# Performance work log

Hardware: AMD Instinct MI355X
Metric: run time of the kernel (lower is better)

Reference implementation:

```python
import jax, jax.numpy as jnp
import numpy as np

N_HEADS = 8
WINDOW = 7

def _conv1x1(x, W, b):
    # x: [B,H,W,C]; 1x1 conv == per-pixel matmul
    return jnp.einsum('bhwc,cd->bhwd', x, W) + b

def _to_heads(t, nh):
    # [B,H,W,C] -> channels-first reshape [B, nh, C//nh, H*W] (matches tf transpose+reshape)
    B, H, W, C = t.shape
    return jnp.transpose(t, (0, 3, 1, 2)).reshape(B, nh, C // nh, H * W)

def setup_inputs() -> dict:
    key = jax.random.key(0)
    ks = jax.random.split(key, 8)
    B, H, W, C = 2, 56, 56, 256
    x = jax.random.normal(ks[0], (B, H, W, C), dtype=jnp.float32)
    s = 1.0 / np.sqrt(C)
    Wq = jax.random.normal(ks[1], (C, C), dtype=jnp.float32) * s
    bq = jnp.zeros((C,), dtype=jnp.float32)
    Wk = jax.random.normal(ks[2], (C, C), dtype=jnp.float32) * s
    bk = jnp.zeros((C,), dtype=jnp.float32)
    Wv = jax.random.normal(ks[3], (C, C), dtype=jnp.float32) * s
    bv = jnp.zeros((C,), dtype=jnp.float32)
    # original initializes gamma to 0 (output == x); use small nonzero so the
    # attention path is observable in outputs/grads
    gamma = jax.random.normal(ks[4], (1,), dtype=jnp.float32) * 0.1
    return {"x": x, "Wq": Wq, "bq": bq, "Wk": Wk, "bk": bk, "Wv": Wv, "bv": bv, "gamma": gamma}

def reference(x, Wq, bq, Wk, bk, Wv, bv, gamma):
    B, H, W, C = x.shape
    p = WINDOW // 2
    xp = jnp.pad(x, ((0, 0), (p, p), (p, p), (0, 0)), mode='reflect')  # [B,Hp,Wp,C]
    q = _to_heads(_conv1x1(x, Wq, bq), N_HEADS)    # [B,nh,dk,HW]
    k = _to_heads(_conv1x1(xp, Wk, bk), N_HEADS)   # [B,nh,dk,HpWp]
    v = _to_heads(_conv1x1(xp, Wv, bv), N_HEADS)   # [B,nh,dk,HpWp]
    energy = jnp.einsum('bhdq,bhdk->bhqk', q, k)   # [B,nh,HW,HpWp]
    attn = jax.nn.softmax(energy, axis=-1)
    out = jnp.einsum('bhdk,bhqk->bhdq', v, attn)   # [B,nh,dk,HW]
    out = out.reshape(B, C, H, W).transpose(0, 2, 3, 1)
    return gamma * out + x
```

## Files before the change

### kernel.cpp

```cpp
#include <hip/hip_runtime.h>

typedef unsigned short u16;
typedef float f32x4 __attribute__((ext_vector_type(4)));
typedef short bf16x8 __attribute__((ext_vector_type(8)));
typedef short bf16x4 __attribute__((ext_vector_type(4)));

__device__ __forceinline__ u16 f2bf(float f) {
    unsigned u = __float_as_uint(f);
    u = (u + 0x7FFFu + ((u >> 16) & 1u)) >> 16;
    return (u16)u;
}

#define LOG2E 1.4426950408889634f

#if __has_builtin(__builtin_amdgcn_exp2f)
__device__ __forceinline__ float exp2_fast(float x) { return __builtin_amdgcn_exp2f(x); }
#else
__device__ __forceinline__ float exp2_fast(float x) { return __expf(x * 0.6931471805599453f); }
#endif

__device__ __forceinline__ unsigned pack2bf(float a, float b) {
    unsigned ua = __float_as_uint(a) + 0x8000u;
    unsigned ub = __float_as_uint(b) + 0x8000u;
#if __has_builtin(__builtin_amdgcn_perm)
    return __builtin_amdgcn_perm(ub, ua, 0x07060302u);
#else
    return ((ua >> 16) & 0xFFFFu) | (ub & 0xFFFF0000u);
#endif
}

#if __has_builtin(__builtin_amdgcn_cvt_pk_bf16_f32)
typedef __bf16 bf2_t __attribute__((ext_vector_type(2)));
__device__ __forceinline__ unsigned cvtpk(float a, float b) {
    bf2_t r = __builtin_amdgcn_cvt_pk_bf16_f32(a, b);
    return __builtin_bit_cast(unsigned, r);
}
#else
__device__ __forceinline__ unsigned cvtpk(float a, float b) { return pack2bf(a, b); }
#endif

__device__ __forceinline__ bf16x4 bc4(uint2 u) { return __builtin_bit_cast(bf16x4, u); }
__device__ __forceinline__ bf16x8 bc8(uint4 u) { return __builtin_bit_cast(bf16x8, u); }

#if __has_builtin(__builtin_amdgcn_global_load_lds)
typedef const __attribute__((address_space(1))) void* as1cv;
typedef __attribute__((address_space(3))) void* as3v;
__device__ __forceinline__ void dma16(const void* g, void* lds_base, int lane) {
    __builtin_amdgcn_global_load_lds((as1cv)g, (as3v)lds_base, 16, 0, 0);
}
#else
__device__ __forceinline__ void dma16(const void* g, void* lds_base, int lane) {
    *(uint4*)((char*)lds_base + lane * 16) = *(const uint4*)g;
}
#endif

#if __has_builtin(__builtin_amdgcn_mfma_f32_16x16x16bf16_1k)
__device__ __forceinline__ f32x4 pv_mfma(bf16x4 a, bf16x4 b, f32x4 c) {
    return __builtin_amdgcn_mfma_f32_16x16x16bf16_1k(a, b, c, 0, 0, 0);
}
#elif __has_builtin(__builtin_amdgcn_mfma_f32_16x16x16_bf16)
__device__ __forceinline__ f32x4 pv_mfma(bf16x4 a, bf16x4 b, f32x4 c) {
    return __builtin_amdgcn_mfma_f32_16x16x16_bf16(a, b, c, 0, 0, 0);
}
#else
__device__ __forceinline__ f32x4 pv_mfma(bf16x4 a, bf16x4 b, f32x4 c) {
    bf16x8 a8 = {a[0], a[1], a[2], a[3], 0, 0, 0, 0};
    bf16x8 b8 = {b[0], b[1], b[2], b[3], 0, 0, 0, 0};
    return __builtin_amdgcn_mfma_f32_16x16x32_bf16(a8, b8, c, 0, 0, 0);
}
#endif

#define BB 2
#define HH 56
#define CC 256
#define NH 8
#define DK 32
#define SQ 3136
#define HP 62
#define SK 3844
#define VT_STRIDE 3856

#define WS_Q    0
#define WS_K    1605632
#define WS_VT   3573760
#define WS_LB   5548032

#define NZERO_F4 413952

#define BSTR 40
__global__ __launch_bounds__(256, 4) void proj_kernel(const float* __restrict__ x,
                                                      const float* __restrict__ Wq,
                                                      const float* __restrict__ Wk,
                                                      const float* __restrict__ Wv,
                                                      const float* __restrict__ bq,
                                                      const float* __restrict__ bk,
                                                      const float* __restrict__ bv,
                                                      u16* __restrict__ qout,
                                                      u16* __restrict__ kout,
                                                      u16* __restrict__ vtout,
                                                      float* __restrict__ out,
                                                      float* __restrict__ lbuf) {
    __shared__ __align__(16) u16 Bl[128 * BSTR];

    int mode  = blockIdx.y;
    int nz    = blockIdx.z;
    int mbase = blockIdx.x * 64;
    int tid = threadIdx.x;

    {
        int gid = ((blockIdx.z * 3 + blockIdx.y) * 121 + blockIdx.x) * 256 + tid;
        const int n_out4 = (SQ * BB * CC) / 4;
        for (int i = gid; i < NZERO_F4; i += 726 * 256) {
            if (i < n_out4) *(float4*)&out[i * 4] = (float4){0.f, 0.f, 0.f, 0.f};
            else            *(float4*)&lbuf[(i - n_out4) * 4] = (float4){0.f, 0.f, 0.f, 0.f};
        }
    }

    int M = (mode == 0) ? (BB * SQ) : (BB * SK);
    if (mbase >= M) return;
    int wave = tid >> 6, lane = tid & 63, quad = lane >> 4, l16 = lane & 15;

    const float* W = (mode == 0) ? Wq : ((mode == 1) ? Wk : Wv);
    const float* bias = (mode == 0) ? bq : ((mode == 1) ? bk : bv);
    float wscale = (mode == 0) ? LOG2E : 1.0f;

    int m_a = mbase + wave * 16 + l16;
    if (m_a >= M) m_a = M - 1;
    int xrow;
    if (mode == 0) {
        xrow = m_a;
    } else {
        int b = (m_a >= SK) ? 1 : 0;
        int sp = m_a - b * SK;
        int hp = sp / HP, wp = sp - hp * HP;
        int hs = hp - 3; hs = hs < 0 ? -hs : (hs >= HH ? 110 - hs : hs);
        int ws_ = wp - 3; ws_ = ws_ < 0 ? -ws_ : (ws_ >= HH ? 110 - ws_ : ws_);
        xrow = b * SQ + hs * HH + ws_;
    }
    const float* xr = x + (size_t)xrow * 256;

    int kq = tid >> 3;
    int cb = (tid & 7) * 16;

    f32x4 acc[8];
#pragma unroll
    for (int i = 0; i < 8; i++) acc[i] = (f32x4){0.f, 0.f, 0.f, 0.f};

    float4 wreg[4];
    auto wload = [&](int s) {
        const float* p = W + (size_t)(s * 32 + kq) * 256 + nz * 128 + cb;
        wreg[0] = *(const float4*)&p[0];
        wreg[1] = *(const float4*)&p[4];
        wreg[2] = *(const float4*)&p[8];
        wreg[3] = *(const float4*)&p[12];
    };
    auto wwrite = [&]() {
#pragma unroll
        for (int i = 0; i < 16; i++) {
            float v = ((const float*)wreg)[i] * wscale;
            Bl[(cb + i) * BSTR + kq] = f2bf(v);
        }
    };

    wload(0);
    for (int s = 0; s < 8; ++s) {
        int kk = s * 32;
        wwrite();
        __syncthreads();
        if (s < 7) wload(s + 1);
        float4 f0 = *(const float4*)&xr[kk + quad * 8];
        float4 f1 = *(const float4*)&xr[kk + quad * 8 + 4];
        uint4 aw = (uint4){pack2bf(f0.x, f0.y), pack2bf(f0.z, f0.w),
                           pack2bf(f1.x, f1.y), pack2bf(f1.z, f1.w)};
        bf16x8 afrag = bc8(aw);
#pragma unroll
        for (int nt = 0; nt < 8; nt++) {
            bf16x8 bfrag = *(const bf16x8*)&Bl[(nt * 16 + l16) * BSTR + quad * 8];
            acc[nt] = __builtin_amdgcn_mfma_f32_16x16x32_bf16(afrag, bfrag, acc[nt], 0, 0, 0);
        }
        __syncthreads();
    }

    int mrow_base = mbase + wave * 16 + quad * 4;
    if (mode == 2) {
#pragma unroll
        for (int nt = 0; nt < 8; nt++) {
            int c = nz * 128 + nt * 16 + l16;
            float bvv = bias[c];
#pragma unroll
            for (int p = 0; p < 4; p += 2) {
                int m = mrow_base + p;
                if (m + 1 < M) {
                    int bb = (m >= SK) ? 1 : 0;
                    int kp = m - bb * SK;
                    unsigned pk = pack2bf(acc[nt][p] + bvv, acc[nt][p + 1] + bvv);
                    *(unsigned*)&vtout[(size_t)(bb * 256 + c) * VT_STRIDE + kp] = pk;
                }
            }
        }
    } else {
#pragma unroll
        for (int r = 0; r < 4; r++) {
            int m = mrow_base + r;
            if (m >= M) continue;
#pragma unroll
            for (int nt = 0; nt < 8; nt++) {
                int c = nz * 128 + nt * 16 + l16;
                float v = acc[nt][r] + bias[c] * ((mode == 0) ? LOG2E : 1.0f);
                u16 hv = f2bf(v);
                if (mode == 0) qout[((size_t)m << 8) + c] = hv;
                else           kout[((size_t)m << 8) + c] = hv;
            }
        }
    }
}

__global__ __launch_bounds__(256) void attn_kernel(const u16* __restrict__ qb,
                                                   const u16* __restrict__ kb,
                                                   const u16* __restrict__ vtb,
                                                   float* __restrict__ out,
                                                   float* __restrict__ lbuf) {
    __shared__ __align__(16) u16 S[16384];

    int tid = threadIdx.x;
    int wave = tid >> 6, lane = tid & 63, quad = lane >> 4, l16 = lane & 15;
    int qs = wave & 1, th = wave >> 1;
    int bh = blockIdx.y;
    int b = bh >> 3, h = bh & 7;
    int half = blockIdx.z;
    int qsub = blockIdx.x * 64 + qs * 32;
    int rounds = half ? 15 : 16;

    bf16x8 qf0 = *(const bf16x8*)&qb[((size_t)(b * SQ + qsub + l16) << 8) + h * 32 + quad * 8];
    bf16x8 qf1 = *(const bf16x8*)&qb[((size_t)(b * SQ + qsub + 16 + l16) << 8) + h * 32 + quad * 8];

    const u16* kg = kb + ((size_t)(b * SK) << 8) + h * 32;
    const u16* vg = vtb + (size_t)(b * 256 + h * 32) * VT_STRIDE;

    f32x4 o00{0.f,0.f,0.f,0.f}, o01{0.f,0.f,0.f,0.f};
    f32x4 o10{0.f,0.f,0.f,0.f}, o11{0.f,0.f,0.f,0.f};
    f32x4 l0{0.f,0.f,0.f,0.f},  l1{0.f,0.f,0.f,0.f};

    short ov = (l16 == 0) ? (short)0x3F80 : (short)0;
    bf16x4 ones4 = {ov, ov, ov, ov};

    auto stage = [&](int r_ch, int buf) {
        u16* base = &S[buf * 8192];
        int kbase = (half * 16 + r_ch) * 128;
#pragma unroll
        for (int i = 0; i < 2; ++i) {
            int g = wave + i * 4;
            int grow = kbase + g * 16 + (lane & 15);
            if (grow > SK - 1) grow = SK - 1;
            dma16(kg + ((size_t)grow << 8) + (lane >> 4) * 8, base + g * 512, lane);
            int col = kbase + (2 * g + (lane >> 5)) * 8;
            if (col > VT_STRIDE - 8) col = VT_STRIDE - 8;
            dma16(vg + (size_t)(lane & 31) * VT_STRIDE + col, base + 4096 + g * 512, lane);
        }
    };

    stage(0, 0);
    __syncthreads();
    stage(1, 1);

    for (int r = 0; r < 16; ++r) {
        if (r < rounds) {
            const u16* Kl = &S[(r & 1) * 8192];
            const u16* Vl = Kl + 4096;
            int ch = half * 16 + r;
            bool tail = (ch == 30);
#pragma unroll
            for (int tt = 0; tt < 4; ++tt) {
                int t = th * 4 + tt;
                bf16x8 kf = *(const bf16x8*)&Kl[t * 512 + ((quad << 4) + l16) * 8];
                f32x4 e0 = __builtin_amdgcn_mfma_f32_16x16x32_bf16(kf, qf0, (f32x4){0.f,0.f,0.f,0.f}, 0, 0, 0);
                f32x4 e1 = __builtin_amdgcn_mfma_f32_16x16x32_bf16(kf, qf1, (f32x4){0.f,0.f,0.f,0.f}, 0, 0, 0);
                float p0[4], p1[4];
                if (tail) {
                    int kb0 = ch * 128 + t * 16 + quad * 4;
#pragma unroll
                    for (int j = 0; j < 4; ++j) {
                        bool valid = (kb0 + j) < SK;
                        p0[j] = valid ? exp2_fast(e0[j]) : 0.f;
                        p1[j] = valid ? exp2_fast(e1[j]) : 0.f;
                    }
                } else {
#pragma unroll
                    for (int j = 0; j < 4; ++j) {
                        p0[j] = exp2_fast(e0[j]);
                        p1[j] = exp2_fast(e1[j]);
                    }
                }
                bf16x4 pa0 = bc4((uint2){cvtpk(p0[0], p0[1]), cvtpk(p0[2], p0[3])});
                bf16x4 pa1 = bc4((uint2){cvtpk(p1[0], p1[1]), cvtpk(p1[2], p1[3])});
                int vbase = ((2 * t + (quad >> 1)) << 8) + (quad & 1) * 4;
                uint2 w0 = *(const uint2*)&Vl[vbase + l16 * 8];
                uint2 w1 = *(const uint2*)&Vl[vbase + (16 + l16) * 8];
                bf16x4 vb0 = bc4(w0), vb1 = bc4(w1);
                o00 = pv_mfma(pa0, vb0, o00);
                o01 = pv_mfma(pa0, vb1, o01);
                o10 = pv_mfma(pa1, vb0, o10);
                o11 = pv_mfma(pa1, vb1, o11);
                l0  = pv_mfma(pa0, ones4, l0);
                l1  = pv_mfma(pa1, ones4, l1);
            }
        }
        __syncthreads();
        if (r + 2 < rounds) stage(r + 2, r & 1);
    }

    float* mg = (float*)&S[0];
    int slot = (qs * 64 + lane) * 24;
    if (th == 1) {
        *(f32x4*)&mg[slot + 0]  = o00;
        *(f32x4*)&mg[slot + 4]  = o01;
        *(f32x4*)&mg[slot + 8]  = o10;
        *(f32x4*)&mg[slot + 12] = o11;
        *(f32x4*)&mg[slot + 16] = l0;
        *(f32x4*)&mg[slot + 20] = l1;
    }
    __syncthreads();
    if (th == 0) {
        o00 += *(const f32x4*)&mg[slot + 0];
        o01 += *(const f32x4*)&mg[slot + 4];
        o10 += *(const f32x4*)&mg[slot + 8];
        o11 += *(const f32x4*)&mg[slot + 12];
        l0  += *(const f32x4*)&mg[slot + 16];
        l1  += *(const f32x4*)&mg[slot + 20];

#pragma unroll
        for (int r2 = 0; r2 < 4; ++r2) {
            int q0 = qsub + quad * 4 + r2;
            int q1 = q0 + 16;
            size_t base0 = (size_t)(b * SQ + q0) * 256 + h * 32;
            size_t base1 = (size_t)(b * SQ + q1) * 256 + h * 32;
            atomicAdd(&out[base0 + l16],      o00[r2]);
            atomicAdd(&out[base0 + 16 + l16], o01[r2]);
            atomicAdd(&out[base1 + l16],      o10[r2]);
            atomicAdd(&out[base1 + 16 + l16], o11[r2]);
            if (l16 == 0) {
                atomicAdd(&lbuf[(b * SQ + q0) * 8 + h], l0[r2]);
                atomicAdd(&lbuf[(b * SQ + q1) * 8 + h], l1[r2]);
            }
        }
    }
}

__global__ __launch_bounds__(256) void finalize_kernel(const float* __restrict__ x,
                                                       const float* __restrict__ gammap,
                                                       const float* __restrict__ lbuf,
                                                       float* __restrict__ out) {
    int gid = blockIdx.x * 256 + threadIdx.x;
    int row = gid >> 6;
    int c4  = (gid & 63) << 2;
    int h   = c4 >> 5;
    float g = gammap[0];
    float linv = g / lbuf[row * 8 + h];
    size_t base = (size_t)row * 256 + c4;
    float4 o = *(const float4*)&out[base];
    float4 xv = *(const float4*)&x[base];
    o.x = o.x * linv + xv.x;
    o.y = o.y * linv + xv.y;
    o.z = o.z * linv + xv.z;
    o.w = o.w * linv + xv.w;
    *(float4*)&out[base] = o;
}

extern "C" void kernel_launch(void* const* d_in, const int* in_sizes, int n_in,
                              void* d_out, int out_size, void* d_ws, size_t ws_size,
                              hipStream_t stream) {
    const float* x     = (const float*)d_in[0];
    const float* Wq    = (const float*)d_in[1];
    const float* bq    = (const float*)d_in[2];
    const float* Wk    = (const float*)d_in[3];
    const float* bk    = (const float*)d_in[4];
    const float* Wv    = (const float*)d_in[5];
    const float* bv    = (const float*)d_in[6];
    const float* gamma = (const float*)d_in[7];
    float* out = (float*)d_out;

    u16* ws   = (u16*)d_ws;
    u16* qbuf = ws + WS_Q;
    u16* kbuf = ws + WS_K;
    u16* vtb  = ws + WS_VT;
    float* lbuf = (float*)(ws + WS_LB);

    proj_kernel<<<dim3(121, 3, 2), 256, 0, stream>>>(x, Wq, Wk, Wv, bq, bk, bv,
                                                     qbuf, kbuf, vtb, out, lbuf);
    attn_kernel<<<dim3(49, 16, 2), 256, 0, stream>>>(qbuf, kbuf, vtb, out, lbuf);
    finalize_kernel<<<1568, 256, 0, stream>>>(x, gamma, lbuf, out);
}
```

Measured before the change: 157.0 us.

## Have each attention wave handle all 64 queries over a quarter of the key tiles

Restructures the attention kernel so each of the four waves covers all 64 queries of the block (four Q fragments) and a disjoint subset of the key tiles, instead of 32 queries and half the key tiles. Each K fragment and V load from LDS is now reused across four query fragments, cutting LDS traffic per MFMA. In exchange it needs more accumulator registers (launch bounds now ask for 4 blocks per CU) and a two-stage LDS reduction across the four waves at the end. The weight-write lambda in the projection kernel is also inlined, with no change in behaviour.

```diff
diff --git a/kernel.cpp b/kernel.cpp
--- a/kernel.cpp
+++ b/kernel.cpp
@@ -154,18 +154,15 @@
         wreg[2] = *(const float4*)&p[8];
         wreg[3] = *(const float4*)&p[12];
     };
-    auto wwrite = [&]() {
+
+    wload(0);
+    for (int s = 0; s < 8; ++s) {
+        int kk = s * 32;
 #pragma unroll
         for (int i = 0; i < 16; i++) {
             float v = ((const float*)wreg)[i] * wscale;
             Bl[(cb + i) * BSTR + kq] = f2bf(v);
         }
-    };
-
-    wload(0);
-    for (int s = 0; s < 8; ++s) {
-        int kk = s * 32;
-        wwrite();
         __syncthreads();
         if (s < 7) wload(s + 1);
         float4 f0 = *(const float4*)&xr[kk + quad * 8];
@@ -215,31 +212,36 @@
     }
 }
 
-__global__ __launch_bounds__(256) void attn_kernel(const u16* __restrict__ qb,
-                                                   const u16* __restrict__ kb,
-                                                   const u16* __restrict__ vtb,
-                                                   float* __restrict__ out,
-                                                   float* __restrict__ lbuf) {
+__global__ __launch_bounds__(256, 4) void attn_kernel(const u16* __restrict__ qb,
+                                                      const u16* __restrict__ kb,
+                                                      const u16* __restrict__ vtb,
+                                                      float* __restrict__ out,
+                                                      float* __restrict__ lbuf) {
     __shared__ __align__(16) u16 S[16384];
 
     int tid = threadIdx.x;
-    int wave = tid >> 6, lane = tid & 63, quad = lane >> 4, l16 = lane & 15;
-    int qs = wave & 1, th = wave >> 1;
+    int th = tid >> 6, lane = tid & 63, quad = lane >> 4, l16 = lane & 15;
     int bh = blockIdx.y;
     int b = bh >> 3, h = bh & 7;
     int half = blockIdx.z;
-    int qsub = blockIdx.x * 64 + qs * 32;
+    int qsub = blockIdx.x * 64;
     int rounds = half ? 15 : 16;
 
-    bf16x8 qf0 = *(const bf16x8*)&qb[((size_t)(b * SQ + qsub + l16) << 8) + h * 32 + quad * 8];
-    bf16x8 qf1 = *(const bf16x8*)&qb[((size_t)(b * SQ + qsub + 16 + l16) << 8) + h * 32 + quad * 8];
+    bf16x8 qf[4];
+#pragma unroll
+    for (int i = 0; i < 4; ++i)
+        qf[i] = *(const bf16x8*)&qb[((size_t)(b * SQ + qsub + i * 16 + l16) << 8) + h * 32 + quad * 8];
 
     const u16* kg = kb + ((size_t)(b * SK) << 8) + h * 32;
     const u16* vg = vtb + (size_t)(b * 256 + h * 32) * VT_STRIDE;
 
-    f32x4 o00{0.f,0.f,0.f,0.f}, o01{0.f,0.f,0.f,0.f};
-    f32x4 o10{0.f,0.f,0.f,0.f}, o11{0.f,0.f,0.f,0.f};
-    f32x4 l0{0.f,0.f,0.f,0.f},  l1{0.f,0.f,0.f,0.f};
+    f32x4 o[4][2], lv[4];
+#pragma unroll
+    for (int i = 0; i < 4; ++i) {
+        o[i][0] = (f32x4){0.f,0.f,0.f,0.f};
+        o[i][1] = (f32x4){0.f,0.f,0.f,0.f};
+        lv[i]   = (f32x4){0.f,0.f,0.f,0.f};
+    }
 
     short ov = (l16 == 0) ? (short)0x3F80 : (short)0;
     bf16x4 ones4 = {ov, ov, ov, ov};
@@ -249,7 +251,7 @@
         int kbase = (half * 16 + r_ch) * 128;
 #pragma unroll
         for (int i = 0; i < 2; ++i) {
-            int g = wave + i * 4;
+            int g = th + i * 4;
             int grow = kbase + g * 16 + (lane & 15);
             if (grow > SK - 1) grow = SK - 1;
             dma16(kg + ((size_t)grow << 8) + (lane >> 4) * 8, base + g * 512, lane);
@@ -263,46 +265,46 @@
     __syncthreads();
     stage(1, 1);
 
-    for (int r = 0; r < 16; ++r) {
-        if (r < rounds) {
-            const u16* Kl = &S[(r & 1) * 8192];
-            const u16* Vl = Kl + 4096;
-            int ch = half * 16 + r;
-            bool tail = (ch == 30);
-#pragma unroll
-            for (int tt = 0; tt < 4; ++tt) {
-                int t = th * 4 + tt;
-                bf16x8 kf = *(const bf16x8*)&Kl[t * 512 + ((quad << 4) + l16) * 8];
-                f32x4 e0 = __builtin_amdgcn_mfma_f32_16x16x32_bf16(kf, qf0, (f32x4){0.f,0.f,0.f,0.f}, 0, 0, 0);
-                f32x4 e1 = __builtin_amdgcn_mfma_f32_16x16x32_bf16(kf, qf1, (f32x4){0.f,0.f,0.f,0.f}, 0, 0, 0);
-                float p0[4], p1[4];
-                if (tail) {
-                    int kb0 = ch * 128 + t * 16 + quad * 4;
-#pragma unroll
-                    for (int j = 0; j < 4; ++j) {
-                        bool valid = (kb0 + j) < SK;
-                        p0[j] = valid ? exp2_fast(e0[j]) : 0.f;
-                        p1[j] = valid ? exp2_fast(e1[j]) : 0.f;
-                    }
-                } else {
-#pragma unroll
-                    for (int j = 0; j < 4; ++j) {
-                        p0[j] = exp2_fast(e0[j]);
-                        p1[j] = exp2_fast(e1[j]);
-                    }
+    for (int r = 0; r < rounds; ++r) {
+        const u16* Kl = &S[(r & 1) * 8192];
+        const u16* Vl = Kl + 4096;
+        int ch = half * 16 + r;
+        bool tail = (ch == 30);
+#pragma unroll
+        for (int tt = 0; tt < 2; ++tt) {
+            int t = th + tt * 4;
+            bf16x8 kf = *(const bf16x8*)&Kl[t * 512 + ((quad << 4) + l16) * 8];
+            f32x4 e[4];
+#pragma unroll
+            for (int i = 0; i < 4; ++i)
+                e[i] = __builtin_amdgcn_mfma_f32_16x16x32_bf16(kf, qf[i], (f32x4){0.f,0.f,0.f,0.f}, 0, 0, 0);
+            bf16x4 pa[4];
+            if (tail) {
+                int kb0 = ch * 128 + t * 16 + quad * 4;
+#pragma unroll
+                for (int i = 0; i < 4; ++i) {
+                    float p0 = (kb0 + 0) < SK ? exp2_fast(e[i][0]) : 0.f;
+                    float p1 = (kb0 + 1) < SK ? exp2_fast(e[i][1]) : 0.f;
+                    float p2 = (kb0 + 2) < SK ? exp2_fast(e[i][2]) : 0.f;
+                    float p3 = (kb0 + 3) < SK ? exp2_fast(e[i][3]) : 0.f;
+                    pa[i] = bc4((uint2){cvtpk(p0, p1), cvtpk(p2, p3)});
                 }
-                bf16x4 pa0 = bc4((uint2){cvtpk(p0[0], p0[1]), cvtpk(p0[2], p0[3])});
-                bf16x4 pa1 = bc4((uint2){cvtpk(p1[0], p1[1]), cvtpk(p1[2], p1[3])});
-                int vbase = ((2 * t + (quad >> 1)) << 8) + (quad & 1) * 4;
-                uint2 w0 = *(const uint2*)&Vl[vbase + l16 * 8];
-                uint2 w1 = *(const uint2*)&Vl[vbase + (16 + l16) * 8];
-                bf16x4 vb0 = bc4(w0), vb1 = bc4(w1);
-                o00 = pv_mfma(pa0, vb0, o00);
-                o01 = pv_mfma(pa0, vb1, o01);
-                o10 = pv_mfma(pa1, vb0, o10);
-                o11 = pv_mfma(pa1, vb1, o11);
-                l0  = pv_mfma(pa0, ones4, l0);
-                l1  = pv_mfma(pa1, ones4, l1);
+            } else {
+#pragma unroll
+                for (int i = 0; i < 4; ++i) {
+                    pa[i] = bc4((uint2){cvtpk(exp2_fast(e[i][0]), exp2_fast(e[i][1])),
+                                        cvtpk(exp2_fast(e[i][2]), exp2_fast(e[i][3]))});
+                }
+            }
+            int vbase = ((2 * t + (quad >> 1)) << 8) + (quad & 1) * 4;
+            uint2 w0 = *(const uint2*)&Vl[vbase + l16 * 8];
+            uint2 w1 = *(const uint2*)&Vl[vbase + (16 + l16) * 8];
+            bf16x4 vb0 = bc4(w0), vb1 = bc4(w1);
+#pragma unroll
+            for (int i = 0; i < 4; ++i) {
+                o[i][0] = pv_mfma(pa[i], vb0, o[i][0]);
+                o[i][1] = pv_mfma(pa[i], vb1, o[i][1]);
+                lv[i]   = pv_mfma(pa[i], ones4, lv[i]);
             }
         }
         __syncthreads();
@@ -310,37 +312,56 @@
     }
 
     float* mg = (float*)&S[0];
-    int slot = (qs * 64 + lane) * 24;
-    if (th == 1) {
-        *(f32x4*)&mg[slot + 0]  = o00;
-        *(f32x4*)&mg[slot + 4]  = o01;
-        *(f32x4*)&mg[slot + 8]  = o10;
-        *(f32x4*)&mg[slot + 12] = o11;
-        *(f32x4*)&mg[slot + 16] = l0;
-        *(f32x4*)&mg[slot + 20] = l1;
-    }
-    __syncthreads();
-    if (th == 0) {
-        o00 += *(const f32x4*)&mg[slot + 0];
-        o01 += *(const f32x4*)&mg[slot + 4];
-        o10 += *(const f32x4*)&mg[slot + 8];
-        o11 += *(const f32x4*)&mg[slot + 12];
-        l0  += *(const f32x4*)&mg[slot + 16];
-        l1  += *(const f32x4*)&mg[slot + 20];
-
-#pragma unroll
-        for (int r2 = 0; r2 < 4; ++r2) {
-            int q0 = qsub + quad * 4 + r2;
-            int q1 = q0 + 16;
-            size_t base0 = (size_t)(b * SQ + q0) * 256 + h * 32;
-            size_t base1 = (size_t)(b * SQ + q1) * 256 + h * 32;
-            atomicAdd(&out[base0 + l16],      o00[r2]);
-            atomicAdd(&out[base0 + 16 + l16], o01[r2]);
-            atomicAdd(&out[base1 + l16],      o10[r2]);
-            atomicAdd(&out[base1 + 16 + l16], o11[r2]);
-            if (l16 == 0) {
-                atomicAdd(&lbuf[(b * SQ + q0) * 8 + h], l0[r2]);
-                atomicAdd(&lbuf[(b * SQ + q1) * 8 + h], l1[r2]);
+    {
+        int slot = ((th & 1) * 64 + lane) * 48;
+        if (th >= 2) {
+#pragma unroll
+            for (int i = 0; i < 4; ++i) {
+                *(f32x4*)&mg[slot + i * 8]     = o[i][0];
+                *(f32x4*)&mg[slot + i * 8 + 4] = o[i][1];
+                *(f32x4*)&mg[slot + 32 + i * 4] = lv[i];
+            }
+        }
+        __syncthreads();
+        if (th < 2) {
+#pragma unroll
+            for (int i = 0; i < 4; ++i) {
+                o[i][0] += *(const f32x4*)&mg[slot + i * 8];
+                o[i][1] += *(const f32x4*)&mg[slot + i * 8 + 4];
+                lv[i]   += *(const f32x4*)&mg[slot + 32 + i * 4];
+            }
+        }
+        __syncthreads();
+    }
+    {
+        int slot = lane * 48;
+        if (th == 1) {
+#pragma unroll
+            for (int i = 0; i < 4; ++i) {
+                *(f32x4*)&mg[slot + i * 8]     = o[i][0];
+                *(f32x4*)&mg[slot + i * 8 + 4] = o[i][1];
+                *(f32x4*)&mg[slot + 32 + i * 4] = lv[i];
+            }
+        }
+        __syncthreads();
+        if (th == 0) {
+#pragma unroll
+            for (int i = 0; i < 4; ++i) {
+                o[i][0] += *(const f32x4*)&mg[slot + i * 8];
+                o[i][1] += *(const f32x4*)&mg[slot + i * 8 + 4];
+                lv[i]   += *(const f32x4*)&mg[slot + 32 + i * 4];
+            }
+
+#pragma unroll
+            for (int i = 0; i < 4; ++i) {
+#pragma unroll
+                for (int r2 = 0; r2 < 4; ++r2) {
+                    int q = qsub + i * 16 + quad * 4 + r2;
+                    size_t base = (size_t)(b * SQ + q) * 256 + h * 32;
+                    atomicAdd(&out[base + l16],      o[i][0][r2]);
+                    atomicAdd(&out[base + 16 + l16], o[i][1][r2]);
+                    if (l16 == 0) atomicAdd(&lbuf[(b * SQ + q) * 8 + h], lv[i][r2]);
+                }
             }
         }
     }
```

After: 156.9 us. About the same (-0.0%).

## Load K/V straight to registers with double-buffering, drop LDS staging

Applied to the files above, without the earlier changes.

The projection kernel now writes V in a tiled layout of 16-key groups per head, so each lane can fetch its MFMA B-fragment directly with one 8-byte global load. The attention kernel drops the LDS double-buffered DMA staging and the per-round barriers. It instead prefetches K and V fragments for the next chunk into registers (A/B ping-pong) while computing the current one. This removes LDS traffic and synchronisation, but raises register pressure and relies on cache for K/V reuse across waves.

```diff
diff --git a/kernel.cpp b/kernel.cpp
--- a/kernel.cpp
+++ b/kernel.cpp
@@ -42,18 +42,6 @@
 __device__ __forceinline__ bf16x4 bc4(uint2 u) { return __builtin_bit_cast(bf16x4, u); }
 __device__ __forceinline__ bf16x8 bc8(uint4 u) { return __builtin_bit_cast(bf16x8, u); }
 
-#if __has_builtin(__builtin_amdgcn_global_load_lds)
-typedef const __attribute__((address_space(1))) void* as1cv;
-typedef __attribute__((address_space(3))) void* as3v;
-__device__ __forceinline__ void dma16(const void* g, void* lds_base, int lane) {
-    __builtin_amdgcn_global_load_lds((as1cv)g, (as3v)lds_base, 16, 0, 0);
-}
-#else
-__device__ __forceinline__ void dma16(const void* g, void* lds_base, int lane) {
-    *(uint4*)((char*)lds_base + lane * 16) = *(const uint4*)g;
-}
-#endif
-
 #if __has_builtin(__builtin_amdgcn_mfma_f32_16x16x16bf16_1k)
 __device__ __forceinline__ f32x4 pv_mfma(bf16x4 a, bf16x4 b, f32x4 c) {
     return __builtin_amdgcn_mfma_f32_16x16x16bf16_1k(a, b, c, 0, 0, 0);
@@ -78,11 +66,11 @@
 #define SQ 3136
 #define HP 62
 #define SK 3844
-#define VT_STRIDE 3856
+#define NTG 241
 
 #define WS_Q    0
 #define WS_K    1605632
-#define WS_VT   3573760
+#define WS_V3   3573760
 #define WS_LB   5548032
 
 #define NZERO_F4 413952
@@ -97,7 +85,7 @@
                                                       const float* __restrict__ bv,
                                                       u16* __restrict__ qout,
                                                       u16* __restrict__ kout,
-                                                      u16* __restrict__ vtout,
+                                                      u16* __restrict__ v3out,
                                                       float* __restrict__ out,
                                                       float* __restrict__ lbuf) {
     __shared__ __align__(16) u16 Bl[128 * BSTR];
@@ -154,18 +142,15 @@
         wreg[2] = *(const float4*)&p[8];
         wreg[3] = *(const float4*)&p[12];
     };
-    auto wwrite = [&]() {
+
+    wload(0);
+    for (int s = 0; s < 8; ++s) {
+        int kk = s * 32;
 #pragma unroll
         for (int i = 0; i < 16; i++) {
             float v = ((const float*)wreg)[i] * wscale;
             Bl[(cb + i) * BSTR + kq] = f2bf(v);
         }
-    };
-
-    wload(0);
-    for (int s = 0; s < 8; ++s) {
-        int kk = s * 32;
-        wwrite();
         __syncthreads();
         if (s < 7) wload(s + 1);
         float4 f0 = *(const float4*)&xr[kk + quad * 8];
@@ -186,6 +171,7 @@
 #pragma unroll
         for (int nt = 0; nt < 8; nt++) {
             int c = nz * 128 + nt * 16 + l16;
+            int hh = c >> 5, dk32 = c & 31;
             float bvv = bias[c];
 #pragma unroll
             for (int p = 0; p < 4; p += 2) {
@@ -193,8 +179,10 @@
                 if (m + 1 < M) {
                     int bb = (m >= SK) ? 1 : 0;
                     int kp = m - bb * SK;
+                    int tg = kp >> 4, ki = kp & 15;
                     unsigned pk = pack2bf(acc[nt][p] + bvv, acc[nt][p + 1] + bvv);
-                    *(unsigned*)&vtout[(size_t)(bb * 256 + c) * VT_STRIDE + kp] = pk;
+                    size_t addr = ((size_t)((bb * 8 + hh) * NTG + tg) << 9) + dk32 * 16 + ki;
+                    *(unsigned*)&v3out[addr] = pk;
                 }
             }
         }
@@ -217,10 +205,10 @@
 
 __global__ __launch_bounds__(256) void attn_kernel(const u16* __restrict__ qb,
                                                    const u16* __restrict__ kb,
-                                                   const u16* __restrict__ vtb,
+                                                   const u16* __restrict__ v3b,
                                                    float* __restrict__ out,
                                                    float* __restrict__ lbuf) {
-    __shared__ __align__(16) u16 S[16384];
+    __shared__ __align__(16) float mg[3072];
 
     int tid = threadIdx.x;
     int wave = tid >> 6, lane = tid & 63, quad = lane >> 4, l16 = lane & 15;
@@ -230,12 +218,13 @@
     int half = blockIdx.z;
     int qsub = blockIdx.x * 64 + qs * 32;
     int rounds = half ? 15 : 16;
+    int ch0 = half * 16;
 
     bf16x8 qf0 = *(const bf16x8*)&qb[((size_t)(b * SQ + qsub + l16) << 8) + h * 32 + quad * 8];
     bf16x8 qf1 = *(const bf16x8*)&qb[((size_t)(b * SQ + qsub + 16 + l16) << 8) + h * 32 + quad * 8];
 
-    const u16* kg = kb + ((size_t)(b * SK) << 8) + h * 32;
-    const u16* vg = vtb + (size_t)(b * 256 + h * 32) * VT_STRIDE;
+    const u16* kg  = kb + ((size_t)(b * SK) << 8) + h * 32;
+    const u16* vgp = v3b + ((size_t)((b * 8 + h) * NTG) << 9);
 
     f32x4 o00{0.f,0.f,0.f,0.f}, o01{0.f,0.f,0.f,0.f};
     f32x4 o10{0.f,0.f,0.f,0.f}, o11{0.f,0.f,0.f,0.f};
@@ -244,72 +233,90 @@
     short ov = (l16 == 0) ? (short)0x3F80 : (short)0;
     bf16x4 ones4 = {ov, ov, ov, ov};
 
-    auto stage = [&](int r_ch, int buf) {
-        u16* base = &S[buf * 8192];
-        int kbase = (half * 16 + r_ch) * 128;
-#pragma unroll
-        for (int i = 0; i < 2; ++i) {
-            int g = wave + i * 4;
-            int grow = kbase + g * 16 + (lane & 15);
-            if (grow > SK - 1) grow = SK - 1;
-            dma16(kg + ((size_t)grow << 8) + (lane >> 4) * 8, base + g * 512, lane);
-            int col = kbase + (2 * g + (lane >> 5)) * 8;
-            if (col > VT_STRIDE - 8) col = VT_STRIDE - 8;
-            dma16(vg + (size_t)(lane & 31) * VT_STRIDE + col, base + 4096 + g * 512, lane);
-        }
-    };
-
-    stage(0, 0);
-    __syncthreads();
-    stage(1, 1);
-
-    for (int r = 0; r < 16; ++r) {
-        if (r < rounds) {
-            const u16* Kl = &S[(r & 1) * 8192];
-            const u16* Vl = Kl + 4096;
-            int ch = half * 16 + r;
-            bool tail = (ch == 30);
-#pragma unroll
-            for (int tt = 0; tt < 4; ++tt) {
-                int t = th * 4 + tt;
-                bf16x8 kf = *(const bf16x8*)&Kl[t * 512 + ((quad << 4) + l16) * 8];
-                f32x4 e0 = __builtin_amdgcn_mfma_f32_16x16x32_bf16(kf, qf0, (f32x4){0.f,0.f,0.f,0.f}, 0, 0, 0);
-                f32x4 e1 = __builtin_amdgcn_mfma_f32_16x16x32_bf16(kf, qf1, (f32x4){0.f,0.f,0.f,0.f}, 0, 0, 0);
-                float p0[4], p1[4];
-                if (tail) {
-                    int kb0 = ch * 128 + t * 16 + quad * 4;
-#pragma unroll
-                    for (int j = 0; j < 4; ++j) {
-                        bool valid = (kb0 + j) < SK;
-                        p0[j] = valid ? exp2_fast(e0[j]) : 0.f;
-                        p1[j] = valid ? exp2_fast(e1[j]) : 0.f;
-                    }
-                } else {
-#pragma unroll
-                    for (int j = 0; j < 4; ++j) {
-                        p0[j] = exp2_fast(e0[j]);
-                        p1[j] = exp2_fast(e1[j]);
-                    }
-                }
-                bf16x4 pa0 = bc4((uint2){cvtpk(p0[0], p0[1]), cvtpk(p0[2], p0[3])});
-                bf16x4 pa1 = bc4((uint2){cvtpk(p1[0], p1[1]), cvtpk(p1[2], p1[3])});
-                int vbase = ((2 * t + (quad >> 1)) << 8) + (quad & 1) * 4;
-                uint2 w0 = *(const uint2*)&Vl[vbase + l16 * 8];
-                uint2 w1 = *(const uint2*)&Vl[vbase + (16 + l16) * 8];
-                bf16x4 vb0 = bc4(w0), vb1 = bc4(w1);
-                o00 = pv_mfma(pa0, vb0, o00);
-                o01 = pv_mfma(pa0, vb1, o01);
-                o10 = pv_mfma(pa1, vb0, o10);
-                o11 = pv_mfma(pa1, vb1, o11);
-                l0  = pv_mfma(pa0, ones4, l0);
-                l1  = pv_mfma(pa1, ones4, l1);
-            }
-        }
-        __syncthreads();
-        if (r + 2 < rounds) stage(r + 2, r & 1);
-    }
-
-    float* mg = (float*)&S[0];
+    auto kptr = [&](int ch, int tt) -> const uint4* {
+        int key = (ch * 8 + th * 4 + tt) * 16 + l16;
+        if (key > SK - 1) key = SK - 1;
+        return (const uint4*)&kg[((size_t)key << 8) + quad * 8];
+    };
+    auto vptr = [&](int ch, int tt, int hi) -> const uint2* {
+        int tg = ch * 8 + th * 4 + tt;
+        if (tg > NTG - 1) tg = NTG - 1;
+        return (const uint2*)&vgp[((size_t)tg << 9) + hi * 256 + l16 * 16 + quad * 4];
+    };
+
+    uint4 kA0, kA1, kA2, kA3, kB0, kB1, kB2, kB3;
+    uint2 vA0l, vA0h, vA1l, vA1h, vA2l, vA2h, vA3l, vA3h;
+    uint2 vB0l, vB0h, vB1l, vB1h, vB2l, vB2h, vB3l, vB3h;
+
+    auto loadA = [&](int ch) {
+        kA0 = *kptr(ch, 0); kA1 = *kptr(ch, 1); kA2 = *kptr(ch, 2); kA3 = *kptr(ch, 3);
+        vA0l = *vptr(ch, 0, 0); vA0h = *vptr(ch, 0, 1);
+        vA1l = *vptr(ch, 1, 0); vA1h = *vptr(ch, 1, 1);
+        vA2l = *vptr(ch, 2, 0); vA2h = *vptr(ch, 2, 1);
+        vA3l = *vptr(ch, 3, 0); vA3h = *vptr(ch, 3, 1);
+    };
+    auto loadB = [&](int ch) {
+        kB0 = *kptr(ch, 0); kB1 = *kptr(ch, 1); kB2 = *kptr(ch, 2); kB3 = *kptr(ch, 3);
+        vB0l = *vptr(ch, 0, 0); vB0h = *vptr(ch, 0, 1);
+        vB1l = *vptr(ch, 1, 0); vB1h = *vptr(ch, 1, 1);
+        vB2l = *vptr(ch, 2, 0); vB2h = *vptr(ch, 2, 1);
+        vB3l = *vptr(ch, 3, 0); vB3h = *vptr(ch, 3, 1);
+    };
+
+    auto compute_tt = [&](int ch, int tt, uint4 kreg, uint2 vlo, uint2 vhi) {
+        bf16x8 kf = bc8(kreg);
+        f32x4 e0 = __builtin_amdgcn_mfma_f32_16x16x32_bf16(kf, qf0, (f32x4){0.f,0.f,0.f,0.f}, 0, 0, 0);
+        f32x4 e1 = __builtin_amdgcn_mfma_f32_16x16x32_bf16(kf, qf1, (f32x4){0.f,0.f,0.f,0.f}, 0, 0, 0);
+        bf16x4 pa0, pa1;
+        if (ch == 30) {
+            int kb0 = (ch * 8 + th * 4 + tt) * 16 + quad * 4;
+            float p00 = (kb0 + 0) < SK ? exp2_fast(e0[0]) : 0.f;
+            float p01 = (kb0 + 1) < SK ? exp2_fast(e0[1]) : 0.f;
+            float p02 = (kb0 + 2) < SK ? exp2_fast(e0[2]) : 0.f;
+            float p03 = (kb0 + 3) < SK ? exp2_fast(e0[3]) : 0.f;
+            float p10 = (kb0 + 0) < SK ? exp2_fast(e1[0]) : 0.f;
+            float p11 = (kb0 + 1) < SK ? exp2_fast(e1[1]) : 0.f;
+            float p12 = (kb0 + 2) < SK ? exp2_fast(e1[2]) : 0.f;
+            float p13 = (kb0 + 3) < SK ? exp2_fast(e1[3]) : 0.f;
+            pa0 = bc4((uint2){cvtpk(p00, p01), cvtpk(p02, p03)});
+            pa1 = bc4((uint2){cvtpk(p10, p11), cvtpk(p12, p13)});
+        } else {
+            pa0 = bc4((uint2){cvtpk(exp2_fast(e0[0]), exp2_fast(e0[1])),
+                              cvtpk(exp2_fast(e0[2]), exp2_fast(e0[3]))});
+            pa1 = bc4((uint2){cvtpk(exp2_fast(e1[0]), exp2_fast(e1[1])),
+                              cvtpk(exp2_fast(e1[2]), exp2_fast(e1[3]))});
+        }
+        bf16x4 vb0 = bc4(vlo), vb1 = bc4(vhi);
+        o00 = pv_mfma(pa0, vb0, o00);
+        o01 = pv_mfma(pa0, vb1, o01);
+        o10 = pv_mfma(pa1, vb0, o10);
+        o11 = pv_mfma(pa1, vb1, o11);
+        l0  = pv_mfma(pa0, ones4, l0);
+        l1  = pv_mfma(pa1, ones4, l1);
+    };
+
+    auto computeA = [&](int ch) {
+        compute_tt(ch, 0, kA0, vA0l, vA0h);
+        compute_tt(ch, 1, kA1, vA1l, vA1h);
+        compute_tt(ch, 2, kA2, vA2l, vA2h);
+        compute_tt(ch, 3, kA3, vA3l, vA3h);
+    };
+    auto computeB = [&](int ch) {
+        compute_tt(ch, 0, kB0, vB0l, vB0h);
+        compute_tt(ch, 1, kB1, vB1l, vB1h);
+        compute_tt(ch, 2, kB2, vB2l, vB2h);
+        compute_tt(ch, 3, kB3, vB3l, vB3h);
+    };
+
+    loadA(ch0);
+    for (int r = 0; r < rounds; r += 2) {
+        if (r + 1 < rounds) loadB(ch0 + r + 1);
+        computeA(ch0 + r);
+        if (r + 1 >= rounds) break;
+        if (r + 2 < rounds) loadA(ch0 + r + 2);
+        computeB(ch0 + r + 1);
+    }
+
     int slot = (qs * 64 + lane) * 24;
     if (th == 1) {
         *(f32x4*)&mg[slot + 0]  = o00;
@@ -382,11 +389,11 @@
     u16* ws   = (u16*)d_ws;
     u16* qbuf = ws + WS_Q;
     u16* kbuf = ws + WS_K;
-    u16* vtb  = ws + WS_VT;
+    u16* v3b  = ws + WS_V3;
     float* lbuf = (float*)(ws + WS_LB);
 
     proj_kernel<<<dim3(121, 3, 2), 256, 0, stream>>>(x, Wq, Wk, Wv, bq, bk, bv,
-                                                     qbuf, kbuf, vtb, out, lbuf);
-    attn_kernel<<<dim3(49, 16, 2), 256, 0, stream>>>(qbuf, kbuf, vtb, out, lbuf);
+                                                     qbuf, kbuf, v3b, out, lbuf);
+    attn_kernel<<<dim3(49, 16, 2), 256, 0, stream>>>(qbuf, kbuf, v3b, out, lbuf);
     finalize_kernel<<<1568, 256, 0, stream>>>(x, gamma, lbuf, out);
 }
```

Measured after the change: 175.7 us. +12.0%, slower.
